# Performance work log

Measured on AMD Instinct MI355X. Metric: run time of the kernel, lower is better.

## Reference

```python
import jax, jax.numpy as jnp
import numpy as np

B, M, N = 8, 512, 1024
D_TS, D_LLM, H, E = 1024, 4096, 16, 64
NEG_INF = float('-inf')


def setup_inputs() -> dict:
    key = jax.random.key(0)
    ks = jax.random.split(key, 12)
    s = 0.02
    return {
        'ts': jax.random.normal(ks[0], (B, M, D_TS), jnp.float32),
        'kv': jax.random.normal(ks[1], (B, N, D_LLM), jnp.float32),
        'ts_mask': jax.random.randint(ks[2], (B, M, 1), 0, 2).astype(jnp.float32),
        'kv_mask': jax.random.randint(ks[3], (B, 1, 1, N), 0, 2).astype(jnp.bool_),
        'Wq': jax.random.normal(ks[4], (D_TS, H * E), jnp.float32) * s,
        'bq': jnp.zeros((H * E,), jnp.float32),
        'Wk': jax.random.normal(ks[5], (D_LLM, H * E), jnp.float32) * s,
        'bk': jnp.zeros((H * E,), jnp.float32),
        'Wv': jax.random.normal(ks[6], (D_LLM, H * E), jnp.float32) * s,
        'bv': jnp.zeros((H * E,), jnp.float32),
        'Wo': jax.random.normal(ks[7], (H * E, D_LLM), jnp.float32) * s,
        'bo': jnp.zeros((D_LLM,), jnp.float32),
    }


def reference(ts, kv, ts_mask, kv_mask, Wq, bq, Wk, bk, Wv, bv, Wo, bo):
    b, m, _ = ts.shape
    n = kv.shape[-2]
    q = (ts @ Wq + bq).reshape(b, m, H, E)   # (B,M,H,E)
    k = (kv @ Wk + bk).reshape(b, n, H, E)   # (B,N,H,E)
    v = (kv @ Wv + bv).reshape(b, n, H, E)
    scores = jnp.einsum('bmhe,bnhe->bhmn', q, k) * (1.0 / np.sqrt(E))
    # masked_fill: True in kv_mask -> -inf
    scores = jnp.where(kv_mask, NEG_INF, scores)
    A = jax.nn.softmax(scores, axis=-1)  # dropout is identity in eval
    out_v = jnp.einsum('bhmn,bnhe->bmhe', A, v).reshape(b, m, H * E)
    out = (out_v @ Wo + bo) * ts_mask
    valid = (ts_mask != 0)[..., 0]  # (B,M)
    scores_for_log = jnp.where(~valid[:, None, :, None], NEG_INF, scores)
    return out, scores_for_log
```

## Files before the change

### kernel.cpp

```cpp
#include <hip/hip_runtime.h>
#include <math.h>

namespace {
constexpr int B_   = 8;
constexpr int M_   = 512;
constexpr int N_   = 1024;
constexpr int DTS  = 1024;
constexpr int DLLM = 4096;
constexpr int H_   = 16;
constexpr int E_   = 64;
constexpr int HE   = H_ * E_;
constexpr float NEG_BIG = -3.0e38f;
}

typedef __attribute__((ext_vector_type(4))) float f32x4;
typedef __attribute__((ext_vector_type(8))) short short8;
typedef unsigned int uint;
typedef unsigned short ushort;

__device__ inline void bsplit(float x, ushort& h, ushort& l) {
  uint u = __float_as_uint(x);
  uint hr = (u + 0x7FFFu + ((u >> 16) & 1u)) & 0xFFFF0000u;
  float lof = x - __uint_as_float(hr);
  h = (ushort)(hr >> 16);
  l = (ushort)(__float_as_uint(lof) >> 16);
}
__device__ inline uint pk(ushort a, ushort b) { return (uint)a | ((uint)b << 16); }

__device__ inline void gld16(const void* g, void* l) {
  __builtin_amdgcn_global_load_lds(
      (const __attribute__((address_space(1))) uint*)g,
      (__attribute__((address_space(3))) uint*)l, 16, 0, 0);
}

__global__ __launch_bounds__(256) void asplit_kernel(
    const float* __restrict__ X, ushort* __restrict__ Xh,
    ushort* __restrict__ Xl, int n8) {
  const int idx = blockIdx.x * 256 + threadIdx.x;
  if (idx >= n8) return;
  const float4 a = *(const float4*)(X + (size_t)idx * 8);
  const float4 b = *(const float4*)(X + (size_t)idx * 8 + 4);
  float f[8] = {a.x, a.y, a.z, a.w, b.x, b.y, b.z, b.w};
  short8 h, l;
#pragma unroll
  for (int j = 0; j < 8; ++j) {
    ushort hh, ll;
    bsplit(f[j], hh, ll);
    h[j] = (short)hh;
    l[j] = (short)ll;
  }
  *(short8*)(Xh + (size_t)idx * 8) = h;
  *(short8*)(Xl + (size_t)idx * 8) = l;
}

__global__ __launch_bounds__(256) void tsplit_kernel(
    const float* __restrict__ W, ushort* __restrict__ Wth,
    ushort* __restrict__ Wtl, int K, int Nc) {
  __shared__ float S[32][33];
  const int t = threadIdx.x;
  const int n0 = blockIdx.x * 32, k0 = blockIdx.y * 32;
  const int c = t & 31, r8 = t >> 5;
#pragma unroll
  for (int i = 0; i < 4; ++i) {
    const int rr = r8 + i * 8;
    S[rr][c] = W[(size_t)(k0 + rr) * Nc + n0 + c];
  }
  __syncthreads();
#pragma unroll
  for (int i = 0; i < 4; ++i) {
    const int nn = r8 + i * 8;
    const float x = S[c][nn];
    ushort h, l;
    bsplit(x, h, l);
    const size_t o = (size_t)(n0 + nn) * K + k0 + c;
    Wth[o] = h;
    Wtl[o] = l;
  }
}

__global__ __launch_bounds__(256) void vtprep_kernel(
    const float* __restrict__ V, ushort* __restrict__ Vth,
    ushort* __restrict__ Vtl) {
  __shared__ float S[64][68];
  const int t  = threadIdx.x;
  const int nt = blockIdx.x & 15;
  const int h  = (blockIdx.x >> 4) & 15;
  const int b  = blockIdx.x >> 8;
  const int n0 = nt * 64;
#pragma unroll
  for (int i = 0; i < 4; ++i) {
    const int idx = i * 256 + t;
    const int row = idx >> 4, c4 = (idx & 15) * 4;
    *(float4*)&S[row][c4] =
        *(const float4*)&V[(size_t)(b * N_ + n0 + row) * HE + h * 64 + c4];
  }
  __syncthreads();
  const int e = t >> 2, nch = (t & 3) * 16;
  short8 h0, h1, l0, l1;
#pragma unroll
  for (int j = 0; j < 8; ++j) {
    ushort hh, ll;
    bsplit(S[nch + j][e], hh, ll);
    h0[j] = (short)hh; l0[j] = (short)ll;
    bsplit(S[nch + 8 + j][e], hh, ll);
    h1[j] = (short)hh; l1[j] = (short)ll;
  }
  const size_t off = (size_t)((b * H_ + h) * 64 + e) * N_ + n0 + nch;
  *(short8*)(Vth + off)     = h0;
  *(short8*)(Vth + off + 8) = h1;
  *(short8*)(Vtl + off)     = l0;
  *(short8*)(Vtl + off + 8) = l1;
}

template <bool ROWMASK, bool SPLITOUT>
__global__ __launch_bounds__(256) void gemm_split3_kernel(
    const float* __restrict__ A, const ushort* __restrict__ Bth,
    const ushort* __restrict__ Btl, const float* __restrict__ bias,
    const float* __restrict__ rowmask, float* __restrict__ C,
    ushort* __restrict__ Ch, ushort* __restrict__ Cl, int Kd, int Nc) {
  __shared__ ushort Ah[128][32];
  __shared__ ushort Al[128][32];
  __shared__ ushort Bh[128][32];
  __shared__ ushort Bl[128][32];

  const int t    = threadIdx.x;
  const int lane = t & 63;
  const int wv   = t >> 6;
  const int l15  = lane & 15;
  const int quad = lane >> 4;
  const int wm   = (wv & 1) * 64;
  const int wn   = (wv >> 1) * 64;
  const int row0 = blockIdx.y * 128;
  const int col0 = blockIdx.x * 128;

  const int arow = t >> 1;
  const int half = t & 1;
  const float* Ap = A + (size_t)(row0 + arow) * Kd + half * 16;

  const int bn  = (lane >> 2);
  const int bk8 = (lane & 3) * 8;
  const ushort* Bhp = Bth + (size_t)(col0 + wv * 32 + bn) * Kd + bk8;
  const ushort* Blp = Btl + (size_t)(col0 + wv * 32 + bn) * Kd + bk8;

  f32x4 acc[4][4];
#pragma unroll
  for (int i = 0; i < 4; ++i)
#pragma unroll
    for (int j = 0; j < 4; ++j) acc[i][j] = {0.f, 0.f, 0.f, 0.f};

  for (int k0 = 0; k0 < Kd; k0 += 32) {
    __syncthreads();
#pragma unroll
    for (int j = 0; j < 2; ++j) {
      const int n = wv * 32 + j * 16 + bn;
      gld16(Bhp + (size_t)j * 16 * Kd + k0, &Bh[n][bk8]);
      gld16(Blp + (size_t)j * 16 * Kd + k0, &Bl[n][bk8]);
    }
    float f[16];
#pragma unroll
    for (int i = 0; i < 4; ++i) {
      const float4 v = *(const float4*)(Ap + k0 + i * 4);
      f[i * 4 + 0] = v.x; f[i * 4 + 1] = v.y;
      f[i * 4 + 2] = v.z; f[i * 4 + 3] = v.w;
    }
    ushort hh[16], ll[16];
#pragma unroll
    for (int i = 0; i < 16; ++i) bsplit(f[i], hh[i], ll[i]);
    uint4 wh0 = {pk(hh[0], hh[1]), pk(hh[2], hh[3]), pk(hh[4], hh[5]), pk(hh[6], hh[7])};
    uint4 wh1 = {pk(hh[8], hh[9]), pk(hh[10], hh[11]), pk(hh[12], hh[13]), pk(hh[14], hh[15])};
    uint4 wl0 = {pk(ll[0], ll[1]), pk(ll[2], ll[3]), pk(ll[4], ll[5]), pk(ll[6], ll[7])};
    uint4 wl1 = {pk(ll[8], ll[9]), pk(ll[10], ll[11]), pk(ll[12], ll[13]), pk(ll[14], ll[15])};
    *(uint4*)&Ah[arow][half * 16 + 0] = wh0;
    *(uint4*)&Ah[arow][half * 16 + 8] = wh1;
    *(uint4*)&Al[arow][half * 16 + 0] = wl0;
    *(uint4*)&Al[arow][half * 16 + 8] = wl1;

    __syncthreads();

    short8 ah[4], al[4], bh[4], bl[4];
#pragma unroll
    for (int mi = 0; mi < 4; ++mi) {
      ah[mi] = *(const short8*)&Ah[wm + mi * 16 + l15][quad * 8];
      al[mi] = *(const short8*)&Al[wm + mi * 16 + l15][quad * 8];
    }
#pragma unroll
    for (int ni = 0; ni < 4; ++ni) {
      bh[ni] = *(const short8*)&Bh[wn + ni * 16 + l15][quad * 8];
      bl[ni] = *(const short8*)&Bl[wn + ni * 16 + l15][quad * 8];
    }
#pragma unroll
    for (int mi = 0; mi < 4; ++mi)
#pragma unroll
      for (int ni = 0; ni < 4; ++ni) {
        acc[mi][ni] = __builtin_amdgcn_mfma_f32_16x16x32_bf16(
            ah[mi], bh[ni], acc[mi][ni], 0, 0, 0);
        acc[mi][ni] = __builtin_amdgcn_mfma_f32_16x16x32_bf16(
            ah[mi], bl[ni], acc[mi][ni], 0, 0, 0);
        acc[mi][ni] = __builtin_amdgcn_mfma_f32_16x16x32_bf16(
            al[mi], bh[ni], acc[mi][ni], 0, 0, 0);
      }
  }

  float bb[4];
#pragma unroll
  for (int ni = 0; ni < 4; ++ni) bb[ni] = bias[col0 + wn + ni * 16 + l15];
#pragma unroll
  for (int mi = 0; mi < 4; ++mi)
#pragma unroll
    for (int r = 0; r < 4; ++r) {
      const int row = row0 + wm + mi * 16 + quad * 4 + r;
      const float rm = ROWMASK ? rowmask[row] : 1.f;
#pragma unroll
      for (int ni = 0; ni < 4; ++ni) {
        const int col = col0 + wn + ni * 16 + l15;
        float v = acc[mi][ni][r] + bb[ni];
        if (SPLITOUT) {
          ushort vh, vl;
          bsplit(v, vh, vl);
          Ch[(size_t)row * Nc + col] = vh;
          Cl[(size_t)row * Nc + col] = vl;
        } else {
          if (ROWMASK) v *= rm;
          C[(size_t)row * Nc + col] = v;
        }
      }
    }
}

template <bool ROWMASK, bool SPLITOUT>
__global__ __launch_bounds__(256) void gemm_bb_kernel(
    const ushort* __restrict__ Ath, const ushort* __restrict__ Atl,
    const ushort* __restrict__ Bth, const ushort* __restrict__ Btl,
    const float* __restrict__ bias, const float* __restrict__ rowmask,
    float* __restrict__ C, ushort* __restrict__ Ch, ushort* __restrict__ Cl,
    int Kd, int Nc, int gx) {
  __shared__ ushort Ah[128][32];
  __shared__ ushort Al[128][32];
  __shared__ ushort Bh[128][32];
  __shared__ ushort Bl[128][32];

  const int t    = threadIdx.x;
  const int lane = t & 63;
  const int wv   = t >> 6;
  const int l15  = lane & 15;
  const int quad = lane >> 4;
  const int wm   = (wv & 1) * 64;
  const int wn   = (wv >> 1) * 64;

  const int lin  = blockIdx.x;
  const int xb   = (lin >> 3) % gx;
  const int yb   = (lin & 7) + 8 * ((lin >> 3) / gx);
  const int row0 = yb * 128;
  const int col0 = xb * 128;

  const int rn  = (lane >> 2);
  const int rk8 = (lane & 3) * 8;
  const ushort* Ahp = Ath + (size_t)(row0 + wv * 32 + rn) * Kd + rk8;
  const ushort* Alp = Atl + (size_t)(row0 + wv * 32 + rn) * Kd + rk8;
  const ushort* Bhp = Bth + (size_t)(col0 + wv * 32 + rn) * Kd + rk8;
  const ushort* Blp = Btl + (size_t)(col0 + wv * 32 + rn) * Kd + rk8;

  f32x4 acc[4][4];
#pragma unroll
  for (int i = 0; i < 4; ++i)
#pragma unroll
    for (int j = 0; j < 4; ++j) acc[i][j] = {0.f, 0.f, 0.f, 0.f};

  for (int k0 = 0; k0 < Kd; k0 += 32) {
    __syncthreads();
#pragma unroll
    for (int j = 0; j < 2; ++j) {
      const int rr = wv * 32 + j * 16;
      const size_t o = (size_t)j * 16 * Kd + k0;
      gld16(Ahp + o, &Ah[rr][0]);
      gld16(Alp + o, &Al[rr][0]);
      gld16(Bhp + o, &Bh[rr][0]);
      gld16(Blp + o, &Bl[rr][0]);
    }
    __syncthreads();

    short8 ah[4], al[4], bh[4], bl[4];
#pragma unroll
    for (int mi = 0; mi < 4; ++mi) {
      ah[mi] = *(const short8*)&Ah[wm + mi * 16 + l15][quad * 8];
      al[mi] = *(const short8*)&Al[wm + mi * 16 + l15][quad * 8];
    }
#pragma unroll
    for (int ni = 0; ni < 4; ++ni) {
      bh[ni] = *(const short8*)&Bh[wn + ni * 16 + l15][quad * 8];
      bl[ni] = *(const short8*)&Bl[wn + ni * 16 + l15][quad * 8];
    }
#pragma unroll
    for (int mi = 0; mi < 4; ++mi)
#pragma unroll
      for (int ni = 0; ni < 4; ++ni) {
        acc[mi][ni] = __builtin_amdgcn_mfma_f32_16x16x32_bf16(
            ah[mi], bh[ni], acc[mi][ni], 0, 0, 0);
        acc[mi][ni] = __builtin_amdgcn_mfma_f32_16x16x32_bf16(
            ah[mi], bl[ni], acc[mi][ni], 0, 0, 0);
        acc[mi][ni] = __builtin_amdgcn_mfma_f32_16x16x32_bf16(
            al[mi], bh[ni], acc[mi][ni], 0, 0, 0);
      }
  }

  float bb[4];
#pragma unroll
  for (int ni = 0; ni < 4; ++ni) bb[ni] = bias[col0 + wn + ni * 16 + l15];
#pragma unroll
  for (int mi = 0; mi < 4; ++mi)
#pragma unroll
    for (int r = 0; r < 4; ++r) {
      const int row = row0 + wm + mi * 16 + quad * 4 + r;
      const float rm = ROWMASK ? rowmask[row] : 1.f;
#pragma unroll
      for (int ni = 0; ni < 4; ++ni) {
        const int col = col0 + wn + ni * 16 + l15;
        float v = acc[mi][ni][r] + bb[ni];
        if (SPLITOUT) {
          ushort vh, vl;
          bsplit(v, vh, vl);
          Ch[(size_t)row * Nc + col] = vh;
          Cl[(size_t)row * Nc + col] = vl;
        } else {
          if (ROWMASK) v *= rm;
          C[(size_t)row * Nc + col] = v;
        }
      }
    }
}

__global__ __launch_bounds__(256) void attn_mfma_kernel(
    const ushort* __restrict__ Qh, const ushort* __restrict__ Ql,
    const ushort* __restrict__ Kh, const ushort* __restrict__ Kl,
    const ushort* __restrict__ Vth, const ushort* __restrict__ Vtl,
    const unsigned char* __restrict__ kvmask, const float* __restrict__ tsmask,
    float* __restrict__ outv, float* __restrict__ scores_out) {
  __shared__ __align__(16) ushort sm[24576];
  ushort* KHT = sm;
  ushort* KLT = sm + 4096;
  ushort* VTH = sm + 8192;
  ushort* VTL = sm + 12288;
  ushort* QHT = sm + 16384;
  ushort* QLT = sm + 20480;

  const int t = threadIdx.x, lane = t & 63, wv = t >> 6;
  const int l15 = lane & 15, quad = lane >> 4;
  const int blk = blockIdx.x;
  const int mt = blk & 7;
  const int h  = (blk >> 3) & 15;
  const int b  = blk >> 7;
  const int m0 = mt * 64;
  const int lrow = lane >> 3, lch = lane & 7;
  const int gch8 = (lch ^ (lrow & 7)) * 8;

#pragma unroll
  for (int i = 0; i < 2; ++i) {
    const int rr = wv * 16 + i * 8;
    const size_t g = (size_t)(b * M_ + m0 + rr + lrow) * HE + h * 64 + gch8;
    gld16(Qh + g, &QHT[rr * 64]);
    gld16(Ql + g, &QLT[rr * 64]);
  }
  __syncthreads();

  short8 qh[2], ql[2];
#pragma unroll
  for (int ks = 0; ks < 2; ++ks) {
    const int row = wv * 16 + l15;
    const int off = row * 64 + (((ks * 4 + quad) ^ (row & 7)) << 3);
    qh[ks] = *(const short8*)&QHT[off];
    ql[ks] = *(const short8*)&QLT[off];
  }
  __builtin_amdgcn_s_waitcnt(0);

  uint* Pu = (uint*)(sm + 16384) + wv * 1024;

  float tsm_v[4];
#pragma unroll
  for (int r = 0; r < 4; ++r)
    tsm_v[r] = tsmask[b * M_ + m0 + wv * 16 + quad * 4 + r];

  float m_i[4] = {-INFINITY, -INFINITY, -INFINITY, -INFINITY};
  float l_i[4] = {0.f, 0.f, 0.f, 0.f};
  f32x4 acc[4];
#pragma unroll
  for (int es = 0; es < 4; ++es) acc[es] = {0.f, 0.f, 0.f, 0.f};

  for (int nc = 0; nc < 16; ++nc) {
    const int n0 = nc * 64;
    __syncthreads();
#pragma unroll
    for (int i = 0; i < 2; ++i) {
      const int rr = wv * 16 + i * 8;
      const size_t gk = (size_t)(b * N_ + n0 + rr + lrow) * HE + h * 64 + gch8;
      const size_t gv = (size_t)((b * H_ + h) * 64 + rr + lrow) * N_ + n0 + gch8;
      gld16(Kh + gk, &KHT[rr * 64]);
      gld16(Kl + gk, &KLT[rr * 64]);
      gld16(Vth + gv, &VTH[rr * 64]);
      gld16(Vtl + gv, &VTL[rr * 64]);
    }
    __syncthreads();

    f32x4 s[4];
#pragma unroll
    for (int ns = 0; ns < 4; ++ns) {
      s[ns] = {0.f, 0.f, 0.f, 0.f};
#pragma unroll
      for (int ks = 0; ks < 2; ++ks) {
        const int row = ns * 16 + l15;
        const int off = row * 64 + (((ks * 4 + quad) ^ (row & 7)) << 3);
        const short8 kh = *(const short8*)&KHT[off];
        const short8 kl = *(const short8*)&KLT[off];
        s[ns] = __builtin_amdgcn_mfma_f32_16x16x32_bf16(qh[ks], kh, s[ns], 0, 0, 0);
        s[ns] = __builtin_amdgcn_mfma_f32_16x16x32_bf16(qh[ks], kl, s[ns], 0, 0, 0);
        s[ns] = __builtin_amdgcn_mfma_f32_16x16x32_bf16(ql[ks], kh, s[ns], 0, 0, 0);
      }
    }

    bool km[4];
#pragma unroll
    for (int ns = 0; ns < 4; ++ns)
      km[ns] = kvmask[b * N_ + n0 + ns * 16 + l15] != 0;
    float sc[4][4];
#pragma unroll
    for (int ns = 0; ns < 4; ++ns)
#pragma unroll
      for (int r = 0; r < 4; ++r)
        sc[r][ns] = km[ns] ? -INFINITY : s[ns][r] * 0.125f;

#pragma unroll
    for (int r = 0; r < 4; ++r) {
      const size_t base =
          ((size_t)(b * H_ + h) * M_ + m0 + wv * 16 + quad * 4 + r) * N_ + n0;
      const bool vr = tsm_v[r] != 0.f;
#pragma unroll
      for (int ns = 0; ns < 4; ++ns)
        scores_out[base + ns * 16 + l15] =
            (vr && !km[ns]) ? sc[r][ns] : NEG_BIG;
    }

#pragma unroll
    for (int r = 0; r < 4; ++r) {
      float cm = fmaxf(fmaxf(sc[r][0], sc[r][1]), fmaxf(sc[r][2], sc[r][3]));
#pragma unroll
      for (int o = 1; o < 16; o <<= 1) cm = fmaxf(cm, __shfl_xor(cm, o));
      const float nm = fmaxf(m_i[r], cm);
      const float alpha = (m_i[r] == -INFINITY) ? 0.f : __expf(m_i[r] - nm);
      float ps = 0.f;
      const int pr = quad * 4 + r;
#pragma unroll
      for (int ns = 0; ns < 4; ++ns) {
        const float p = (sc[r][ns] == -INFINITY) ? 0.f : __expf(sc[r][ns] - nm);
        ps += p;
        ushort ph_, pl_;
        bsplit(p, ph_, pl_);
        const int c = ns * 16 + l15;
        Pu[pr * 64 + (((c >> 2) ^ (pr & 7)) << 2) + (c & 3)] = pk(ph_, pl_);
      }
#pragma unroll
      for (int o = 1; o < 16; o <<= 1) ps += __shfl_xor(ps, o);
      l_i[r] = l_i[r] * alpha + ps;
      m_i[r] = nm;
#pragma unroll
      for (int es = 0; es < 4; ++es) acc[es][r] *= alpha;
    }

#pragma unroll
    for (int ks = 0; ks < 2; ++ks) {
      const int c0 = ks * 8 + quad * 2;
      const uint* pb = &Pu[l15 * 64];
      const uint4 u0 = *(const uint4*)&pb[(c0 ^ (l15 & 7)) << 2];
      const uint4 u1 = *(const uint4*)&pb[((c0 + 1) ^ (l15 & 7)) << 2];
      short8 ph, pl;
      const uint* up0 = (const uint*)&u0;
      const uint* up1 = (const uint*)&u1;
#pragma unroll
      for (int j = 0; j < 4; ++j) {
        ph[j] = (short)(up0[j] & 0xffffu); pl[j] = (short)(up0[j] >> 16);
        ph[4 + j] = (short)(up1[j] & 0xffffu); pl[4 + j] = (short)(up1[j] >> 16);
      }
#pragma unroll
      for (int es = 0; es < 4; ++es) {
        const int row = es * 16 + l15;
        const int off = row * 64 + (((ks * 4 + quad) ^ (row & 7)) << 3);
        const short8 vh = *(const short8*)&VTH[off];
        const short8 vl = *(const short8*)&VTL[off];
        acc[es] = __builtin_amdgcn_mfma_f32_16x16x32_bf16(ph, vh, acc[es], 0, 0, 0);
        acc[es] = __builtin_amdgcn_mfma_f32_16x16x32_bf16(ph, vl, acc[es], 0, 0, 0);
        acc[es] = __builtin_amdgcn_mfma_f32_16x16x32_bf16(pl, vh, acc[es], 0, 0, 0);
      }
    }
  }

#pragma unroll
  for (int r = 0; r < 4; ++r) {
    const float inv = (l_i[r] > 0.f) ? 1.f / l_i[r] : 0.f;
    const int grow = b * M_ + m0 + wv * 16 + quad * 4 + r;
#pragma unroll
    for (int es = 0; es < 4; ++es)
      outv[(size_t)grow * HE + h * 64 + es * 16 + l15] = acc[es][r] * inv;
  }
}

extern "C" void kernel_launch(void* const* d_in, const int* in_sizes, int n_in,
                              void* d_out, int out_size, void* d_ws,
                              size_t ws_size, hipStream_t stream) {
  const float* ts  = (const float*)d_in[0];
  const float* kv  = (const float*)d_in[1];
  const float* tsm = (const float*)d_in[2];
  const unsigned char* kvm = (const unsigned char*)d_in[3];
  const float* Wq = (const float*)d_in[4];
  const float* bq = (const float*)d_in[5];
  const float* Wk = (const float*)d_in[6];
  const float* bk = (const float*)d_in[7];
  const float* Wv = (const float*)d_in[8];
  const float* bv = (const float*)d_in[9];
  const float* Wo = (const float*)d_in[10];
  const float* bo = (const float*)d_in[11];

  float* out        = (float*)d_out;
  float* scores_out = out + (size_t)B_ * M_ * DLLM;

  char* ws = (char*)d_ws;
  constexpr size_t MB = 1024 * 1024;

  if (ws_size >= 260 * MB) {
    ushort* Kvh  = (ushort*)(ws);
    ushort* Kvl  = (ushort*)(ws + 64 * MB);
    float*  Vf   = (float*)(ws + 128 * MB);
    ushort* Khp  = (ushort*)(ws + 160 * MB);
    ushort* Klp  = (ushort*)(ws + 176 * MB);
    ushort* Qhp  = (ushort*)(ws + 192 * MB);
    ushort* Qlp  = (ushort*)(ws + 200 * MB);
    ushort* Tsh  = (ushort*)(ws + 208 * MB);
    ushort* Tsl  = (ushort*)(ws + 216 * MB);
    ushort* Wqh  = (ushort*)(ws + 224 * MB);
    ushort* Wql  = (ushort*)(ws + 226 * MB);
    ushort* Wkh  = (ushort*)(ws + 228 * MB);
    ushort* Wkl  = (ushort*)(ws + 236 * MB);
    ushort* Wvh  = (ushort*)(ws + 244 * MB);
    ushort* Wvl  = (ushort*)(ws + 252 * MB);
    ushort* Vthp  = (ushort*)(ws);
    ushort* Vtlp  = (ushort*)(ws + 16 * MB);
    ushort* outvh = (ushort*)(ws + 32 * MB);
    ushort* outvl = (ushort*)(ws + 40 * MB);
    ushort* Woh   = (ushort*)(ws + 64 * MB);
    ushort* Wol   = (ushort*)(ws + 72 * MB);
    float*  outv  = (float*)(ws + 128 * MB);

    {
      const int n8_ts = (B_ * M_ * DTS) / 8;
      asplit_kernel<<<dim3(n8_ts / 256), 256, 0, stream>>>(ts, Tsh, Tsl, n8_ts);
      const int n8_kv = (B_ * N_ * DLLM) / 8;
      asplit_kernel<<<dim3(n8_kv / 256), 256, 0, stream>>>(kv, Kvh, Kvl, n8_kv);
    }

    tsplit_kernel<<<dim3(HE / 32, DTS / 32), 256, 0, stream>>>(Wq, Wqh, Wql, DTS, HE);
    tsplit_kernel<<<dim3(HE / 32, DLLM / 32), 256, 0, stream>>>(Wk, Wkh, Wkl, DLLM, HE);
    tsplit_kernel<<<dim3(HE / 32, DLLM / 32), 256, 0, stream>>>(Wv, Wvh, Wvl, DLLM, HE);

    gemm_bb_kernel<false, true><<<dim3((HE / 128) * ((B_ * M_) / 128)), 256, 0, stream>>>(
        Tsh, Tsl, Wqh, Wql, bq, nullptr, nullptr, Qhp, Qlp, DTS, HE, HE / 128);
    gemm_bb_kernel<false, true><<<dim3((HE / 128) * ((B_ * N_) / 128)), 256, 0, stream>>>(
        Kvh, Kvl, Wkh, Wkl, bk, nullptr, nullptr, Khp, Klp, DLLM, HE, HE / 128);
    gemm_bb_kernel<false, false><<<dim3((HE / 128) * ((B_ * N_) / 128)), 256, 0, stream>>>(
        Kvh, Kvl, Wvh, Wvl, bv, nullptr, Vf, nullptr, nullptr, DLLM, HE, HE / 128);

    vtprep_kernel<<<dim3(B_ * H_ * 16), 256, 0, stream>>>(Vf, Vthp, Vtlp);

    attn_mfma_kernel<<<dim3(B_ * H_ * (M_ / 64)), 256, 0, stream>>>(
        Qhp, Qlp, Khp, Klp, Vthp, Vtlp, kvm, tsm, outv, scores_out);

    {
      const int n8_o = (B_ * M_ * HE) / 8;
      asplit_kernel<<<dim3(n8_o / 256), 256, 0, stream>>>(outv, outvh, outvl, n8_o);
    }

    tsplit_kernel<<<dim3(DLLM / 32, HE / 32), 256, 0, stream>>>(Wo, Woh, Wol, HE, DLLM);
    gemm_bb_kernel<true, false><<<dim3((DLLM / 128) * ((B_ * M_) / 128)), 256, 0, stream>>>(
        outvh, outvl, Woh, Wol, bo, tsm, out, nullptr, nullptr, HE, DLLM, DLLM / 128);
  } else {
    float*  Vf   = (float*)(ws);
    float*  outv = (float*)(ws);
    ushort* Qhp  = (ushort*)(ws + 32 * MB);
    ushort* Qlp  = (ushort*)(ws + 40 * MB);
    ushort* Khp  = (ushort*)(ws + 48 * MB);
    ushort* Klp  = (ushort*)(ws + 64 * MB);
    ushort* Wqh  = (ushort*)(ws + 80 * MB);
    ushort* Wql  = (ushort*)(ws + 82 * MB);
    ushort* Wkh  = (ushort*)(ws + 84 * MB);
    ushort* Wkl  = (ushort*)(ws + 92 * MB);
    ushort* Wvh  = (ushort*)(ws + 100 * MB);
    ushort* Wvl  = (ushort*)(ws + 108 * MB);
    ushort* Vthp = (ushort*)(ws + 84 * MB);
    ushort* Vtlp = (ushort*)(ws + 100 * MB);
    ushort* Woh  = (ushort*)(ws + 48 * MB);
    ushort* Wol  = (ushort*)(ws + 56 * MB);

    tsplit_kernel<<<dim3(HE / 32, DTS / 32), 256, 0, stream>>>(Wq, Wqh, Wql, DTS, HE);
    tsplit_kernel<<<dim3(HE / 32, DLLM / 32), 256, 0, stream>>>(Wk, Wkh, Wkl, DLLM, HE);
    tsplit_kernel<<<dim3(HE / 32, DLLM / 32), 256, 0, stream>>>(Wv, Wvh, Wvl, DLLM, HE);

    gemm_split3_kernel<false, true><<<dim3(HE / 128, (B_ * M_) / 128), 256, 0, stream>>>(
        ts, Wqh, Wql, bq, nullptr, nullptr, Qhp, Qlp, DTS, HE);
    gemm_split3_kernel<false, true><<<dim3(HE / 128, (B_ * N_) / 128), 256, 0, stream>>>(
        kv, Wkh, Wkl, bk, nullptr, nullptr, Khp, Klp, DLLM, HE);
    gemm_split3_kernel<false, false><<<dim3(HE / 128, (B_ * N_) / 128), 256, 0, stream>>>(
        kv, Wvh, Wvl, bv, nullptr, Vf, nullptr, nullptr, DLLM, HE);

    vtprep_kernel<<<dim3(B_ * H_ * 16), 256, 0, stream>>>(Vf, Vthp, Vtlp);

    attn_mfma_kernel<<<dim3(B_ * H_ * (M_ / 64)), 256, 0, stream>>>(
        Qhp, Qlp, Khp, Klp, Vthp, Vtlp, kvm, tsm, outv, scores_out);

    tsplit_kernel<<<dim3(DLLM / 32, HE / 32), 256, 0, stream>>>(Wo, Woh, Wol, HE, DLLM);
    gemm_split3_kernel<true, false><<<dim3(DLLM / 128, (B_ * M_) / 128), 256, 0, stream>>>(
        outv, Woh, Wol, bo, tsm, out, nullptr, nullptr, HE, DLLM);
  }
}
```

Before: 1.245 ms.

## Double-buffer LDS tiles in bf16x3 GEMM to overlap global loads with MFMA

Converts the split-bf16 GEMM main loop to double-buffered shared memory. The next K-slab is prefetched into the alternate buffer, and partial vmcnt waits let those loads run while the MFMAs work on the current slab. Raw s_barrier, sched_barrier and s_setprio calls control ordering and raise wave priority during the MFMA block. Shared memory per block doubles, which may reduce occupancy, and the hand-counted vmcnt value must match the number of async loads issued.

```diff
diff --git a/kernel.cpp b/kernel.cpp
--- a/kernel.cpp
+++ b/kernel.cpp
@@ -234,10 +234,10 @@
     const float* __restrict__ bias, const float* __restrict__ rowmask,
     float* __restrict__ C, ushort* __restrict__ Ch, ushort* __restrict__ Cl,
     int Kd, int Nc, int gx) {
-  __shared__ ushort Ah[128][32];
-  __shared__ ushort Al[128][32];
-  __shared__ ushort Bh[128][32];
-  __shared__ ushort Bl[128][32];
+  __shared__ ushort Ah[2][128][32];
+  __shared__ ushort Al[2][128][32];
+  __shared__ ushort Bh[2][128][32];
+  __shared__ ushort Bl[2][128][32];
 
   const int t    = threadIdx.x;
   const int lane = t & 63;
@@ -266,30 +266,50 @@
 #pragma unroll
     for (int j = 0; j < 4; ++j) acc[i][j] = {0.f, 0.f, 0.f, 0.f};
 
+#pragma unroll
+  for (int j = 0; j < 2; ++j) {
+    const int rr = wv * 32 + j * 16;
+    const size_t o = (size_t)j * 16 * Kd;
+    gld16(Ahp + o, &Ah[0][rr][0]);
+    gld16(Alp + o, &Al[0][rr][0]);
+    gld16(Bhp + o, &Bh[0][rr][0]);
+    gld16(Blp + o, &Bl[0][rr][0]);
+  }
+
+  int cur = 0;
   for (int k0 = 0; k0 < Kd; k0 += 32) {
-    __syncthreads();
-#pragma unroll
-    for (int j = 0; j < 2; ++j) {
-      const int rr = wv * 32 + j * 16;
-      const size_t o = (size_t)j * 16 * Kd + k0;
-      gld16(Ahp + o, &Ah[rr][0]);
-      gld16(Alp + o, &Al[rr][0]);
-      gld16(Bhp + o, &Bh[rr][0]);
-      gld16(Blp + o, &Bl[rr][0]);
-    }
-    __syncthreads();
+    const bool has_next = (k0 + 32 < Kd);
+    if (has_next) {
+      const int nb = cur ^ 1;
+#pragma unroll
+      for (int j = 0; j < 2; ++j) {
+        const int rr = wv * 32 + j * 16;
+        const size_t o = (size_t)j * 16 * Kd + k0 + 32;
+        gld16(Ahp + o, &Ah[nb][rr][0]);
+        gld16(Alp + o, &Al[nb][rr][0]);
+        gld16(Bhp + o, &Bh[nb][rr][0]);
+        gld16(Blp + o, &Bl[nb][rr][0]);
+      }
+      asm volatile("s_waitcnt vmcnt(8)" ::: "memory");
+    } else {
+      asm volatile("s_waitcnt vmcnt(0)" ::: "memory");
+    }
+    __builtin_amdgcn_sched_barrier(0);
+    __builtin_amdgcn_s_barrier();
+    __builtin_amdgcn_sched_barrier(0);
 
     short8 ah[4], al[4], bh[4], bl[4];
 #pragma unroll
     for (int mi = 0; mi < 4; ++mi) {
-      ah[mi] = *(const short8*)&Ah[wm + mi * 16 + l15][quad * 8];
-      al[mi] = *(const short8*)&Al[wm + mi * 16 + l15][quad * 8];
+      ah[mi] = *(const short8*)&Ah[cur][wm + mi * 16 + l15][quad * 8];
+      al[mi] = *(const short8*)&Al[cur][wm + mi * 16 + l15][quad * 8];
     }
 #pragma unroll
     for (int ni = 0; ni < 4; ++ni) {
-      bh[ni] = *(const short8*)&Bh[wn + ni * 16 + l15][quad * 8];
-      bl[ni] = *(const short8*)&Bl[wn + ni * 16 + l15][quad * 8];
-    }
+      bh[ni] = *(const short8*)&Bh[cur][wn + ni * 16 + l15][quad * 8];
+      bl[ni] = *(const short8*)&Bl[cur][wn + ni * 16 + l15][quad * 8];
+    }
+    __builtin_amdgcn_s_setprio(1);
 #pragma unroll
     for (int mi = 0; mi < 4; ++mi)
 #pragma unroll
@@ -301,6 +321,13 @@
         acc[mi][ni] = __builtin_amdgcn_mfma_f32_16x16x32_bf16(
             al[mi], bh[ni], acc[mi][ni], 0, 0, 0);
       }
+    __builtin_amdgcn_s_setprio(0);
+
+    __builtin_amdgcn_sched_barrier(0);
+    asm volatile("s_waitcnt lgkmcnt(0)" ::: "memory");
+    __builtin_amdgcn_s_barrier();
+    __builtin_amdgcn_sched_barrier(0);
+    cur ^= 1;
   }
 
   float bb[4];
```

After: 1.239 ms. Within noise of the previous version (-0.5%).

## Load GEMM B operand directly to registers with double-buffered prefetch and swizzled LDS

Applied to the files above, without the earlier changes.

The split-bf16 GEMM now loads the B (weight) fragments straight from global memory into registers, double-buffered one k-step ahead, and only stages A through LDS, using an XOR swizzle to avoid bank conflicts. Manual waitcnt and barriers plus setprio around the MFMA block are meant to overlap global loads with compute and halve LDS traffic. Register pressure rises, and the inline-asm vmcnt(8) accounting assumes a fixed number of outstanding loads, so it is fragile. The last iteration also prefetches k=0 again, which is wasted work.

```diff
diff --git a/kernel.cpp b/kernel.cpp
--- a/kernel.cpp
+++ b/kernel.cpp
@@ -31,6 +31,11 @@
   __builtin_amdgcn_global_load_lds(
       (const __attribute__((address_space(1))) uint*)g,
       (__attribute__((address_space(3))) uint*)l, 16, 0, 0);
+}
+
+__device__ __forceinline__ void gload16(short8& d, const ushort* p) {
+  asm volatile("global_load_dwordx4 %0, %1, off"
+               : "=v"(d) : "v"(p) : "memory");
 }
 
 __global__ __launch_bounds__(256) void asplit_kernel(
@@ -227,8 +232,62 @@
     }
 }
 
+#define LOADB8(SH, SL, KK)          \
+  gload16(SH[0], bhp0 + (KK));      \
+  gload16(SH[1], bhp1 + (KK));      \
+  gload16(SH[2], bhp2 + (KK));      \
+  gload16(SH[3], bhp3 + (KK));      \
+  gload16(SL[0], blp0 + (KK));      \
+  gload16(SL[1], blp1 + (KK));      \
+  gload16(SL[2], blp2 + (KK));      \
+  gload16(SL[3], blp3 + (KK));
+
+#define STAGEA(KK)                                      \
+  _Pragma("unroll")                                     \
+  for (int j = 0; j < 2; ++j) {                         \
+    const int rr = wv * 32 + j * 16;                    \
+    const size_t o = (size_t)j * 16 * Kd + (KK);        \
+    gld16(Ahp + o, &Ah[rr][0]);                         \
+    gld16(Alp + o, &Al[rr][0]);                         \
+  }
+
+#define SYNC_TOP()                                      \
+  asm volatile("s_waitcnt vmcnt(8)" ::: "memory");      \
+  __builtin_amdgcn_sched_barrier(0);                    \
+  __builtin_amdgcn_s_barrier();                         \
+  __builtin_amdgcn_sched_barrier(0);
+
+#define SYNC_BOT()                                      \
+  __builtin_amdgcn_sched_barrier(0);                    \
+  asm volatile("s_waitcnt lgkmcnt(0)" ::: "memory");    \
+  __builtin_amdgcn_s_barrier();                         \
+  __builtin_amdgcn_sched_barrier(0);
+
+#define COMPUTE(BH, BL)                                                     \
+  {                                                                         \
+    short8 ah[4], al[4];                                                    \
+    _Pragma("unroll")                                                       \
+    for (int mi = 0; mi < 4; ++mi) {                                        \
+      ah[mi] = *(const short8*)&Ah[wm + mi * 16 + l15][fsw];                \
+      al[mi] = *(const short8*)&Al[wm + mi * 16 + l15][fsw];                \
+    }                                                                       \
+    __builtin_amdgcn_s_setprio(1);                                          \
+    _Pragma("unroll")                                                       \
+    for (int mi = 0; mi < 4; ++mi)                                          \
+      _Pragma("unroll")                                                     \
+      for (int ni = 0; ni < 4; ++ni) {                                      \
+        acc[mi][ni] = __builtin_amdgcn_mfma_f32_16x16x32_bf16(              \
+            ah[mi], BH[ni], acc[mi][ni], 0, 0, 0);                          \
+        acc[mi][ni] = __builtin_amdgcn_mfma_f32_16x16x32_bf16(              \
+            ah[mi], BL[ni], acc[mi][ni], 0, 0, 0);                          \
+        acc[mi][ni] = __builtin_amdgcn_mfma_f32_16x16x32_bf16(              \
+            al[mi], BH[ni], acc[mi][ni], 0, 0, 0);                          \
+      }                                                                     \
+    __builtin_amdgcn_s_setprio(0);                                          \
+  }
+
 template <bool ROWMASK, bool SPLITOUT>
-__global__ __launch_bounds__(256) void gemm_bb_kernel(
+__global__ __launch_bounds__(256) void gemm_breg_kernel(
     const ushort* __restrict__ Ath, const ushort* __restrict__ Atl,
     const ushort* __restrict__ Bth, const ushort* __restrict__ Btl,
     const float* __restrict__ bias, const float* __restrict__ rowmask,
@@ -236,8 +295,6 @@
     int Kd, int Nc, int gx) {
   __shared__ ushort Ah[128][32];
   __shared__ ushort Al[128][32];
-  __shared__ ushort Bh[128][32];
-  __shared__ ushort Bl[128][32];
 
   const int t    = threadIdx.x;
   const int lane = t & 63;
@@ -253,12 +310,21 @@
   const int row0 = yb * 128;
   const int col0 = xb * 128;
 
-  const int rn  = (lane >> 2);
-  const int rk8 = (lane & 3) * 8;
-  const ushort* Ahp = Ath + (size_t)(row0 + wv * 32 + rn) * Kd + rk8;
-  const ushort* Alp = Atl + (size_t)(row0 + wv * 32 + rn) * Kd + rk8;
-  const ushort* Bhp = Bth + (size_t)(col0 + wv * 32 + rn) * Kd + rk8;
-  const ushort* Blp = Btl + (size_t)(col0 + wv * 32 + rn) * Kd + rk8;
+  const int srow = lane >> 2;
+  const int sch8 = ((lane & 3) ^ (srow & 3)) * 8;
+  const ushort* Ahp = Ath + (size_t)(row0 + wv * 32 + srow) * Kd + sch8;
+  const ushort* Alp = Atl + (size_t)(row0 + wv * 32 + srow) * Kd + sch8;
+
+  const int fsw = (quad ^ (l15 & 3)) * 8;
+
+  const ushort* bhp0 = Bth + (size_t)(col0 + wn +  0 + l15) * Kd + quad * 8;
+  const ushort* bhp1 = Bth + (size_t)(col0 + wn + 16 + l15) * Kd + quad * 8;
+  const ushort* bhp2 = Bth + (size_t)(col0 + wn + 32 + l15) * Kd + quad * 8;
+  const ushort* bhp3 = Bth + (size_t)(col0 + wn + 48 + l15) * Kd + quad * 8;
+  const ushort* blp0 = Btl + (size_t)(col0 + wn +  0 + l15) * Kd + quad * 8;
+  const ushort* blp1 = Btl + (size_t)(col0 + wn + 16 + l15) * Kd + quad * 8;
+  const ushort* blp2 = Btl + (size_t)(col0 + wn + 32 + l15) * Kd + quad * 8;
+  const ushort* blp3 = Btl + (size_t)(col0 + wn + 48 + l15) * Kd + quad * 8;
 
   f32x4 acc[4][4];
 #pragma unroll
@@ -266,41 +332,23 @@
 #pragma unroll
     for (int j = 0; j < 4; ++j) acc[i][j] = {0.f, 0.f, 0.f, 0.f};
 
-  for (int k0 = 0; k0 < Kd; k0 += 32) {
-    __syncthreads();
-#pragma unroll
-    for (int j = 0; j < 2; ++j) {
-      const int rr = wv * 32 + j * 16;
-      const size_t o = (size_t)j * 16 * Kd + k0;
-      gld16(Ahp + o, &Ah[rr][0]);
-      gld16(Alp + o, &Al[rr][0]);
-      gld16(Bhp + o, &Bh[rr][0]);
-      gld16(Blp + o, &Bl[rr][0]);
-    }
-    __syncthreads();
-
-    short8 ah[4], al[4], bh[4], bl[4];
-#pragma unroll
-    for (int mi = 0; mi < 4; ++mi) {
-      ah[mi] = *(const short8*)&Ah[wm + mi * 16 + l15][quad * 8];
-      al[mi] = *(const short8*)&Al[wm + mi * 16 + l15][quad * 8];
-    }
-#pragma unroll
-    for (int ni = 0; ni < 4; ++ni) {
-      bh[ni] = *(const short8*)&Bh[wn + ni * 16 + l15][quad * 8];
-      bl[ni] = *(const short8*)&Bl[wn + ni * 16 + l15][quad * 8];
-    }
-#pragma unroll
-    for (int mi = 0; mi < 4; ++mi)
-#pragma unroll
-      for (int ni = 0; ni < 4; ++ni) {
-        acc[mi][ni] = __builtin_amdgcn_mfma_f32_16x16x32_bf16(
-            ah[mi], bh[ni], acc[mi][ni], 0, 0, 0);
-        acc[mi][ni] = __builtin_amdgcn_mfma_f32_16x16x32_bf16(
-            ah[mi], bl[ni], acc[mi][ni], 0, 0, 0);
-        acc[mi][ni] = __builtin_amdgcn_mfma_f32_16x16x32_bf16(
-            al[mi], bh[ni], acc[mi][ni], 0, 0, 0);
-      }
+  short8 b0h[4], b0l[4], b1h[4], b1l[4];
+
+  LOADB8(b0h, b0l, 0);
+
+  for (int k0 = 0; k0 < Kd; k0 += 64) {
+    STAGEA(k0);
+    LOADB8(b1h, b1l, k0 + 32);
+    SYNC_TOP();
+    COMPUTE(b0h, b0l);
+    SYNC_BOT();
+
+    STAGEA(k0 + 32);
+    const int kn = (k0 + 64 < Kd) ? k0 + 64 : 0;
+    LOADB8(b0h, b0l, kn);
+    SYNC_TOP();
+    COMPUTE(b1h, b1l);
+    SYNC_BOT();
   }
 
   float bb[4];
@@ -328,6 +376,12 @@
       }
     }
 }
+
+#undef LOADB8
+#undef STAGEA
+#undef SYNC_TOP
+#undef SYNC_BOT
+#undef COMPUTE
 
 __global__ __launch_bounds__(256) void attn_mfma_kernel(
     const ushort* __restrict__ Qh, const ushort* __restrict__ Ql,
@@ -558,11 +612,11 @@
     tsplit_kernel<<<dim3(HE / 32, DLLM / 32), 256, 0, stream>>>(Wk, Wkh, Wkl, DLLM, HE);
     tsplit_kernel<<<dim3(HE / 32, DLLM / 32), 256, 0, stream>>>(Wv, Wvh, Wvl, DLLM, HE);
 
-    gemm_bb_kernel<false, true><<<dim3((HE / 128) * ((B_ * M_) / 128)), 256, 0, stream>>>(
+    gemm_breg_kernel<false, true><<<dim3((HE / 128) * ((B_ * M_) / 128)), 256, 0, stream>>>(
         Tsh, Tsl, Wqh, Wql, bq, nullptr, nullptr, Qhp, Qlp, DTS, HE, HE / 128);
-    gemm_bb_kernel<false, true><<<dim3((HE / 128) * ((B_ * N_) / 128)), 256, 0, stream>>>(
+    gemm_breg_kernel<false, true><<<dim3((HE / 128) * ((B_ * N_) / 128)), 256, 0, stream>>>(
         Kvh, Kvl, Wkh, Wkl, bk, nullptr, nullptr, Khp, Klp, DLLM, HE, HE / 128);
-    gemm_bb_kernel<false, false><<<dim3((HE / 128) * ((B_ * N_) / 128)), 256, 0, stream>>>(
+    gemm_breg_kernel<false, false><<<dim3((HE / 128) * ((B_ * N_) / 128)), 256, 0, stream>>>(
         Kvh, Kvl, Wvh, Wvl, bv, nullptr, Vf, nullptr, nullptr, DLLM, HE, HE / 128);
 
     vtprep_kernel<<<dim3(B_ * H_ * 16), 256, 0, stream>>>(Vf, Vthp, Vtlp);
@@ -576,7 +630,7 @@
     }
 
     tsplit_kernel<<<dim3(DLLM / 32, HE / 32), 256, 0, stream>>>(Wo, Woh, Wol, HE, DLLM);
-    gemm_bb_kernel<true, false><<<dim3((DLLM / 128) * ((B_ * M_) / 128)), 256, 0, stream>>>(
+    gemm_breg_kernel<true, false><<<dim3((DLLM / 128) * ((B_ * M_) / 128)), 256, 0, stream>>>(
         outvh, outvl, Woh, Wol, bo, tsm, out, nullptr, nullptr, HE, DLLM, DLLM / 128);
   } else {
     float*  Vf   = (float*)(ws);
```

New measurement: 1.465 ms. 17.7% more time.

## Split-K the K and V projection GEMMs and fuse the partial reduction

Applied to the files above, without the earlier changes.

The K and V projections (K=4096) now run as a split-K GEMM with two K halves, doubling the grid so more blocks run concurrently. Each half writes fp32 partials into the scores output buffer, which is used as scratch before attention overwrites it. A combine kernel adds the partials and bias and does the bf16 hi/lo split for K, and a fused vtprep2 kernel does the same plus the transpose for V. The trade is extra partial-sum memory traffic and two small kernels in exchange for better occupancy on the long-K GEMMs.

```diff
diff --git a/kernel.cpp b/kernel.cpp
--- a/kernel.cpp
+++ b/kernel.cpp
@@ -11,6 +11,7 @@
 constexpr int E_   = 64;
 constexpr int HE   = H_ * E_;
 constexpr float NEG_BIG = -3.0e38f;
+constexpr size_t PST = (size_t)8192 * 1024;
 }
 
 typedef __attribute__((ext_vector_type(4))) float f32x4;
@@ -53,6 +54,35 @@
   *(short8*)(Xl + (size_t)idx * 8) = l;
 }
 
+__global__ __launch_bounds__(256) void kcombine_kernel(
+    const float* __restrict__ P0, const float* __restrict__ P1,
+    const float* __restrict__ bias, ushort* __restrict__ Ch,
+    ushort* __restrict__ Cl, int Nc) {
+  const int idx = blockIdx.x * 256 + threadIdx.x;
+  const size_t base = (size_t)idx * 8;
+  const int col = (int)(base & (size_t)(Nc - 1));
+  const float4 a0 = *(const float4*)(P0 + base);
+  const float4 a1 = *(const float4*)(P0 + base + 4);
+  const float4 b0 = *(const float4*)(P1 + base);
+  const float4 b1 = *(const float4*)(P1 + base + 4);
+  const float4 c0 = *(const float4*)(bias + col);
+  const float4 c1 = *(const float4*)(bias + col + 4);
+  float f[8] = {a0.x + b0.x + c0.x, a0.y + b0.y + c0.y,
+                a0.z + b0.z + c0.z, a0.w + b0.w + c0.w,
+                a1.x + b1.x + c1.x, a1.y + b1.y + c1.y,
+                a1.z + b1.z + c1.z, a1.w + b1.w + c1.w};
+  short8 h, l;
+#pragma unroll
+  for (int j = 0; j < 8; ++j) {
+    ushort hh, ll;
+    bsplit(f[j], hh, ll);
+    h[j] = (short)hh;
+    l[j] = (short)ll;
+  }
+  *(short8*)(Ch + base) = h;
+  *(short8*)(Cl + base) = l;
+}
+
 __global__ __launch_bounds__(256) void tsplit_kernel(
     const float* __restrict__ W, ushort* __restrict__ Wth,
     ushort* __restrict__ Wtl, int K, int Nc) {
@@ -76,6 +106,49 @@
     Wth[o] = h;
     Wtl[o] = l;
   }
+}
+
+__global__ __launch_bounds__(256) void vtprep2_kernel(
+    const float* __restrict__ P0, const float* __restrict__ P1,
+    const float* __restrict__ bias, ushort* __restrict__ Vth,
+    ushort* __restrict__ Vtl) {
+  __shared__ float S[64][68];
+  const int t  = threadIdx.x;
+  const int nt = blockIdx.x & 15;
+  const int h  = (blockIdx.x >> 4) & 15;
+  const int b  = blockIdx.x >> 8;
+  const int n0 = nt * 64;
+#pragma unroll
+  for (int i = 0; i < 4; ++i) {
+    const int idx = i * 256 + t;
+    const int row = idx >> 4, c4 = (idx & 15) * 4;
+    const size_t go = (size_t)(b * N_ + n0 + row) * HE + h * 64 + c4;
+    const float4 v0 = *(const float4*)(P0 + go);
+    const float4 v1 = *(const float4*)(P1 + go);
+    const float4 bb = *(const float4*)(bias + h * 64 + c4);
+    float4 s;
+    s.x = v0.x + v1.x + bb.x;
+    s.y = v0.y + v1.y + bb.y;
+    s.z = v0.z + v1.z + bb.z;
+    s.w = v0.w + v1.w + bb.w;
+    *(float4*)&S[row][c4] = s;
+  }
+  __syncthreads();
+  const int e = t >> 2, nch = (t & 3) * 16;
+  short8 h0, h1, l0, l1;
+#pragma unroll
+  for (int j = 0; j < 8; ++j) {
+    ushort hh, ll;
+    bsplit(S[nch + j][e], hh, ll);
+    h0[j] = (short)hh; l0[j] = (short)ll;
+    bsplit(S[nch + 8 + j][e], hh, ll);
+    h1[j] = (short)hh; l1[j] = (short)ll;
+  }
+  const size_t off = (size_t)((b * H_ + h) * 64 + e) * N_ + n0 + nch;
+  *(short8*)(Vth + off)     = h0;
+  *(short8*)(Vth + off + 8) = h1;
+  *(short8*)(Vtl + off)     = l0;
+  *(short8*)(Vtl + off + 8) = l1;
 }
 
 __global__ __launch_bounds__(256) void vtprep_kernel(
@@ -325,6 +398,96 @@
           if (ROWMASK) v *= rm;
           C[(size_t)row * Nc + col] = v;
         }
+      }
+    }
+}
+
+__global__ __launch_bounds__(256) void gemm_part_kernel(
+    const ushort* __restrict__ Ath, const ushort* __restrict__ Atl,
+    const ushort* __restrict__ Bth, const ushort* __restrict__ Btl,
+    float* __restrict__ Cpart, int Kd, int KH, int Nc, int gx) {
+  __shared__ ushort Ah[128][32];
+  __shared__ ushort Al[128][32];
+  __shared__ ushort Bh[128][32];
+  __shared__ ushort Bl[128][32];
+
+  const int t    = threadIdx.x;
+  const int lane = t & 63;
+  const int wv   = t >> 6;
+  const int l15  = lane & 15;
+  const int quad = lane >> 4;
+  const int wm   = (wv & 1) * 64;
+  const int wn   = (wv >> 1) * 64;
+
+  const int lin  = blockIdx.x;
+  const int ks   = lin & 1;
+  const int rest = lin >> 1;
+  const int xb   = (rest >> 3) % gx;
+  const int yb   = (rest & 7) + 8 * ((rest >> 3) / gx);
+  const int row0 = yb * 128;
+  const int col0 = xb * 128;
+
+  const int rn  = (lane >> 2);
+  const int rk8 = (lane & 3) * 8;
+  const ushort* Ahp = Ath + (size_t)(row0 + wv * 32 + rn) * Kd + rk8;
+  const ushort* Alp = Atl + (size_t)(row0 + wv * 32 + rn) * Kd + rk8;
+  const ushort* Bhp = Bth + (size_t)(col0 + wv * 32 + rn) * Kd + rk8;
+  const ushort* Blp = Btl + (size_t)(col0 + wv * 32 + rn) * Kd + rk8;
+
+  f32x4 acc[4][4];
+#pragma unroll
+  for (int i = 0; i < 4; ++i)
+#pragma unroll
+    for (int j = 0; j < 4; ++j) acc[i][j] = {0.f, 0.f, 0.f, 0.f};
+
+  const int kbeg = ks * KH;
+  for (int k0 = kbeg; k0 < kbeg + KH; k0 += 32) {
+    __syncthreads();
+#pragma unroll
+    for (int j = 0; j < 2; ++j) {
+      const int rr = wv * 32 + j * 16;
+      const size_t o = (size_t)j * 16 * Kd + k0;
+      gld16(Ahp + o, &Ah[rr][0]);
+      gld16(Alp + o, &Al[rr][0]);
+      gld16(Bhp + o, &Bh[rr][0]);
+      gld16(Blp + o, &Bl[rr][0]);
+    }
+    __syncthreads();
+
+    short8 ah[4], al[4], bh[4], bl[4];
+#pragma unroll
+    for (int mi = 0; mi < 4; ++mi) {
+      ah[mi] = *(const short8*)&Ah[wm + mi * 16 + l15][quad * 8];
+      al[mi] = *(const short8*)&Al[wm + mi * 16 + l15][quad * 8];
+    }
+#pragma unroll
+    for (int ni = 0; ni < 4; ++ni) {
+      bh[ni] = *(const short8*)&Bh[wn + ni * 16 + l15][quad * 8];
+      bl[ni] = *(const short8*)&Bl[wn + ni * 16 + l15][quad * 8];
+    }
+#pragma unroll
+    for (int mi = 0; mi < 4; ++mi)
+#pragma unroll
+      for (int ni = 0; ni < 4; ++ni) {
+        acc[mi][ni] = __builtin_amdgcn_mfma_f32_16x16x32_bf16(
+            ah[mi], bh[ni], acc[mi][ni], 0, 0, 0);
+        acc[mi][ni] = __builtin_amdgcn_mfma_f32_16x16x32_bf16(
+            ah[mi], bl[ni], acc[mi][ni], 0, 0, 0);
+        acc[mi][ni] = __builtin_amdgcn_mfma_f32_16x16x32_bf16(
+            al[mi], bh[ni], acc[mi][ni], 0, 0, 0);
+      }
+  }
+
+  float* Cp = Cpart + (size_t)ks * PST;
+#pragma unroll
+  for (int mi = 0; mi < 4; ++mi)
+#pragma unroll
+    for (int r = 0; r < 4; ++r) {
+      const int row = row0 + wm + mi * 16 + quad * 4 + r;
+#pragma unroll
+      for (int ni = 0; ni < 4; ++ni) {
+        const int col = col0 + wn + ni * 16 + l15;
+        Cp[(size_t)row * Nc + col] = acc[mi][ni][r];
       }
     }
 }
@@ -526,7 +689,6 @@
   if (ws_size >= 260 * MB) {
     ushort* Kvh  = (ushort*)(ws);
     ushort* Kvl  = (ushort*)(ws + 64 * MB);
-    float*  Vf   = (float*)(ws + 128 * MB);
     ushort* Khp  = (ushort*)(ws + 160 * MB);
     ushort* Klp  = (ushort*)(ws + 176 * MB);
     ushort* Qhp  = (ushort*)(ws + 192 * MB);
@@ -547,6 +709,9 @@
     ushort* Wol   = (ushort*)(ws + 72 * MB);
     float*  outv  = (float*)(ws + 128 * MB);
 
+    float* Kp = scores_out;
+    float* Vp = scores_out + 2 * PST;
+
     {
       const int n8_ts = (B_ * M_ * DTS) / 8;
       asplit_kernel<<<dim3(n8_ts / 256), 256, 0, stream>>>(ts, Tsh, Tsl, n8_ts);
@@ -560,12 +725,17 @@
 
     gemm_bb_kernel<false, true><<<dim3((HE / 128) * ((B_ * M_) / 128)), 256, 0, stream>>>(
         Tsh, Tsl, Wqh, Wql, bq, nullptr, nullptr, Qhp, Qlp, DTS, HE, HE / 128);
-    gemm_bb_kernel<false, true><<<dim3((HE / 128) * ((B_ * N_) / 128)), 256, 0, stream>>>(
-        Kvh, Kvl, Wkh, Wkl, bk, nullptr, nullptr, Khp, Klp, DLLM, HE, HE / 128);
-    gemm_bb_kernel<false, false><<<dim3((HE / 128) * ((B_ * N_) / 128)), 256, 0, stream>>>(
-        Kvh, Kvl, Wvh, Wvl, bv, nullptr, Vf, nullptr, nullptr, DLLM, HE, HE / 128);
-
-    vtprep_kernel<<<dim3(B_ * H_ * 16), 256, 0, stream>>>(Vf, Vthp, Vtlp);
+
+    gemm_part_kernel<<<dim3(2 * (HE / 128) * ((B_ * N_) / 128)), 256, 0, stream>>>(
+        Kvh, Kvl, Wkh, Wkl, Kp, DLLM, DLLM / 2, HE, HE / 128);
+    gemm_part_kernel<<<dim3(2 * (HE / 128) * ((B_ * N_) / 128)), 256, 0, stream>>>(
+        Kvh, Kvl, Wvh, Wvl, Vp, DLLM, DLLM / 2, HE, HE / 128);
+
+    kcombine_kernel<<<dim3((B_ * N_ * HE / 8) / 256), 256, 0, stream>>>(
+        Kp, Kp + PST, bk, Khp, Klp, HE);
+
+    vtprep2_kernel<<<dim3(B_ * H_ * 16), 256, 0, stream>>>(
+        Vp, Vp + PST, bv, Vthp, Vtlp);
 
     attn_mfma_kernel<<<dim3(B_ * H_ * (M_ / 64)), 256, 0, stream>>>(
         Qhp, Qlp, Khp, Klp, Vthp, Vtlp, kvm, tsm, outv, scores_out);
```

Result: slower. 1.275 ms (+2.4%).
